# Kernel tuning notes

Measured on AMD Instinct MI355X. Metric: run time of the kernel, lower is better.

Reference implementation:

```python
import jax, jax.numpy as jnp
import numpy as np


def _jacobian_circulant(v):
    """Spatial Jacobian of a 3D vector field with circulant boundaries.

    v : (B, X, Y, Z, D) velocity field (channels last)
    returns J : (B, X, Y, Z, D, D) with J[..., i, j] = d v_i / d x_j,
    computed by central differences with wrap-around (circulant) bounds.
    """
    cols = []
    for j in range(3):
        ax = 1 + j  # spatial axis for coordinate j
        g = (jnp.roll(v, -1, axis=ax) - jnp.roll(v, 1, axis=ax)) * 0.5
        cols.append(g)
    return jnp.stack(cols, axis=-1)  # (B, X, Y, Z, D, D)


def _bracket(x, y):
    """Lie bracket of two velocity fields: [x, y] = J_x y - J_y x."""
    jx = _jacobian_circulant(x)
    jy = _jacobian_circulant(y)
    return (jnp.einsum('bxyzij,bxyzj->bxyzi', jx, y)
            - jnp.einsum('bxyzij,bxyzj->bxyzi', jy, x))


def _bch(x, y, trunc=2):
    """Truncated BCH series: z s.t. exp(z) = exp(x) o exp(y)."""
    z = x + y
    if trunc >= 2:
        z = z + 0.5 * _bracket(x, y)
    return z


def setup_inputs() -> dict:
    key = jax.random.key(0)
    k1, k2 = jax.random.split(key)
    B, D, X, Y, Z = 2, 3, 128, 128, 128
    left = jax.random.normal(k1, (B, D, X, Y, Z), dtype=jnp.float32)
    right = jax.random.normal(k2, (B, D, X, Y, Z), dtype=jnp.float32)
    return {"left": left, "right": right}


def reference(left, right):
    # (B, D, *shape) -> channels-last (B, *shape, D)
    l = jnp.moveaxis(left, 1, -1)
    r = jnp.moveaxis(right, 1, -1)
    v = _bch(l, r, trunc=2)
    return jnp.moveaxis(v, -1, 1)
```

## Files before the change

kernel.cpp:

```cpp
#include <hip/hip_runtime.h>


namespace {
constexpr int Xd = 128, Yd = 128, Zd = 128, Bd = 2, Dd = 3;
constexpr int Sd  = Xd * Yd * Zd;
constexpr int YZd = Yd * Zd;

__device__ inline float4 f4sub(float4 a, float4 b) {
    return make_float4(a.x - b.x, a.y - b.y, a.z - b.z, a.w - b.w);
}
__device__ inline float4 f4add(float4 a, float4 b) {
    return make_float4(a.x + b.x, a.y + b.y, a.z + b.z, a.w + b.w);
}
__device__ inline float4 f4mul(float4 a, float4 b) {
    return make_float4(a.x * b.x, a.y * b.y, a.z * b.z, a.w * b.w);
}
__device__ inline float4 f4fma(float4 a, float4 b, float4 c) {
    return make_float4(fmaf(a.x, b.x, c.x), fmaf(a.y, b.y, c.y),
                       fmaf(a.z, b.z, c.z), fmaf(a.w, b.w, c.w));
}
__device__ inline float4 f4fms(float4 a, float4 b, float4 c) {
    return make_float4(fmaf(-a.x, b.x, c.x), fmaf(-a.y, b.y, c.y),
                       fmaf(-a.z, b.z, c.z), fmaf(-a.w, b.w, c.w));
}
}

__global__ void __launch_bounds__(256)
bch_kernel(const float* __restrict__ L, const float* __restrict__ R,
           float* __restrict__ O)
{
    const int tid = blockIdx.x * 256 + threadIdx.x;
    const int z0  = (tid & 31) << 2;
    int t = tid >> 5;
    const int y = t & 127; t >>= 7;
    const int x = t & 127;
    const int b = t >> 7;

    const int base = b * (Dd * Sd) + x * YZd + y * Zd + z0;

    const int oxp = (((x + 1) & 127) - x) * YZd;
    const int oxm = (((x - 1) & 127) - x) * YZd;
    const int oyp = (((y + 1) & 127) - y) * Zd;
    const int oym = (((y - 1) & 127) - y) * Zd;
    const int ozm = ((z0 - 1) & 127) - z0;
    const int ozp = ((z0 + 4) & 127) - z0;

    float4 Lc[3], Rc[3];
#pragma unroll
    for (int d = 0; d < 3; ++d) {
        Lc[d] = *(const float4*)(L + base + d * Sd);
        Rc[d] = *(const float4*)(R + base + d * Sd);
    }

#pragma unroll
    for (int i = 0; i < 3; ++i) {
        const float* lp = L + base + i * Sd;
        const float* rp = R + base + i * Sd;

        float4 dl = f4sub(*(const float4*)(lp + oxp), *(const float4*)(lp + oxm));
        float4 dr = f4sub(*(const float4*)(rp + oxp), *(const float4*)(rp + oxm));
        float4 br = f4fms(dr, Lc[0], f4mul(dl, Rc[0]));

        dl = f4sub(*(const float4*)(lp + oyp), *(const float4*)(lp + oym));
        dr = f4sub(*(const float4*)(rp + oyp), *(const float4*)(rp + oym));
        br = f4fms(dr, Lc[1], f4fma(dl, Rc[1], br));

        const float lzm = lp[ozm], lzp = lp[ozp];
        const float rzm = rp[ozm], rzp = rp[ozp];
        dl = make_float4(Lc[i].y - lzm, Lc[i].z - Lc[i].x,
                         Lc[i].w - Lc[i].y, lzp - Lc[i].z);
        dr = make_float4(Rc[i].y - rzm, Rc[i].z - Rc[i].x,
                         Rc[i].w - Rc[i].y, rzp - Rc[i].z);
        br = f4fms(dr, Lc[2], f4fma(dl, Rc[2], br));

        float4 out = f4add(Lc[i], Rc[i]);
        const float4 q = make_float4(0.25f, 0.25f, 0.25f, 0.25f);
        out = f4fma(q, br, out);

        *(float4*)(O + base + i * Sd) = out;
    }
}

extern "C" void kernel_launch(void* const* d_in, const int* in_sizes, int n_in,
                              void* d_out, int out_size, void* d_ws, size_t ws_size,
                              hipStream_t stream)
{
    const float* L = (const float*)d_in[0];
    const float* R = (const float*)d_in[1];
    float*       O = (float*)d_out;

    const int nthreads = Bd * Xd * Yd * (Zd / 4);
    dim3 grid(nthreads / 256), block(256);
    bch_kernel<<<grid, block, 0, stream>>>(L, R, O);
}
```

Measured before the change: 152.2 us.

## March along y with register sliding window and warp shuffles for z neighbors

```diff
diff --git a/kernel.cpp b/kernel.cpp
--- a/kernel.cpp
+++ b/kernel.cpp
@@ -2,18 +2,17 @@
 
 
 namespace {
-constexpr int Xd = 128, Yd = 128, Zd = 128, Bd = 2, Dd = 3;
-constexpr int Sd  = Xd * Yd * Zd;
-constexpr int YZd = Yd * Zd;
+constexpr int NB = 2, ND = 3, NX = 128, NY = 128, NZ = 128;
+constexpr int XS = NY * NZ;
+constexpr int YSEG = 8;
+
+__device__ inline float4 ld4(const float* p) { return *(const float4*)p; }
 
 __device__ inline float4 f4sub(float4 a, float4 b) {
     return make_float4(a.x - b.x, a.y - b.y, a.z - b.z, a.w - b.w);
 }
 __device__ inline float4 f4add(float4 a, float4 b) {
     return make_float4(a.x + b.x, a.y + b.y, a.z + b.z, a.w + b.w);
-}
-__device__ inline float4 f4mul(float4 a, float4 b) {
-    return make_float4(a.x * b.x, a.y * b.y, a.z * b.z, a.w * b.w);
 }
 __device__ inline float4 f4fma(float4 a, float4 b, float4 c) {
     return make_float4(fmaf(a.x, b.x, c.x), fmaf(a.y, b.y, c.y),
@@ -23,61 +22,101 @@
     return make_float4(fmaf(-a.x, b.x, c.x), fmaf(-a.y, b.y, c.y),
                        fmaf(-a.z, b.z, c.z), fmaf(-a.w, b.w, c.w));
 }
+__device__ inline float4 f4mul(float4 a, float4 b) {
+    return make_float4(a.x * b.x, a.y * b.y, a.z * b.z, a.w * b.w);
+}
+
+__device__ inline float4 zderiv(float4 c, int srcm, int srcp) {
+    const float lw = __shfl(c.w, srcm, 64);
+    const float rx = __shfl(c.x, srcp, 64);
+    return make_float4(c.y - lw, c.z - c.x, c.w - c.y, rx - c.z);
+}
 }
 
 __global__ void __launch_bounds__(256)
 bch_kernel(const float* __restrict__ L, const float* __restrict__ R,
            float* __restrict__ O)
 {
-    const int tid = blockIdx.x * 256 + threadIdx.x;
-    const int z0  = (tid & 31) << 2;
-    int t = tid >> 5;
-    const int y = t & 127; t >>= 7;
-    const int x = t & 127;
-    const int b = t >> 7;
+    const int lane = threadIdx.x & 31;
+    const int g    = blockIdx.x * 8 + (threadIdx.x >> 5);
+    const int yseg = g & 15;
+    const int x    = (g >> 4) & 127;
+    const int b    = g >> 11;
+    const int z0   = lane << 2;
+    const int y0   = yseg * YSEG;
 
-    const int base = b * (Dd * Sd) + x * YZd + y * Zd + z0;
+    const int wl   = threadIdx.x & 63;
+    const int srcm = (wl & 32) | ((wl + 31) & 31);
+    const int srcp = (wl & 32) | ((wl + 1) & 31);
 
-    const int oxp = (((x + 1) & 127) - x) * YZd;
-    const int oxm = (((x - 1) & 127) - x) * YZd;
-    const int oyp = (((y + 1) & 127) - y) * Zd;
-    const int oym = (((y - 1) & 127) - y) * Zd;
-    const int ozm = ((z0 - 1) & 127) - z0;
-    const int ozp = ((z0 + 4) & 127) - z0;
-
-    float4 Lc[3], Rc[3];
+    int offc[3], offxp[3], offxm[3];
+    const int xp = (x + 1) & 127, xm = (x - 1) & 127;
 #pragma unroll
-    for (int d = 0; d < 3; ++d) {
-        Lc[d] = *(const float4*)(L + base + d * Sd);
-        Rc[d] = *(const float4*)(R + base + d * Sd);
+    for (int c = 0; c < 3; ++c) {
+        const int bc = (b * 3 + c) * NX;
+        offc[c]  = (bc + x)  * XS + z0;
+        offxp[c] = (bc + xp) * XS + z0;
+        offxm[c] = (bc + xm) * XS + z0;
     }
 
+    float4 Lm[3], Lc[3], Rm[3], Rc[3];
+    {
+        const int ymo = ((y0 + 127) & 127) * NZ;
+        const int yco = y0 * NZ;
 #pragma unroll
-    for (int i = 0; i < 3; ++i) {
-        const float* lp = L + base + i * Sd;
-        const float* rp = R + base + i * Sd;
+        for (int c = 0; c < 3; ++c) {
+            Lm[c] = ld4(L + offc[c] + ymo);
+            Rm[c] = ld4(R + offc[c] + ymo);
+            Lc[c] = ld4(L + offc[c] + yco);
+            Rc[c] = ld4(R + offc[c] + yco);
+        }
+    }
 
-        float4 dl = f4sub(*(const float4*)(lp + oxp), *(const float4*)(lp + oxm));
-        float4 dr = f4sub(*(const float4*)(rp + oxp), *(const float4*)(rp + oxm));
-        float4 br = f4fms(dr, Lc[0], f4mul(dl, Rc[0]));
+    for (int it = 0; it < YSEG; ++it) {
+        const int y  = y0 + it;
+        const int yr = y * NZ;
+        const int yp = ((y + 1) & 127) * NZ;
 
-        dl = f4sub(*(const float4*)(lp + oyp), *(const float4*)(lp + oym));
-        dr = f4sub(*(const float4*)(rp + oyp), *(const float4*)(rp + oym));
-        br = f4fms(dr, Lc[1], f4fma(dl, Rc[1], br));
+        float4 Lp[3], Rp[3], LxP[3], LxM[3], RxP[3], RxM[3];
+#pragma unroll
+        for (int c = 0; c < 3; ++c) {
+            Lp[c]  = ld4(L + offc[c]  + yp);
+            Rp[c]  = ld4(R + offc[c]  + yp);
+            LxP[c] = ld4(L + offxp[c] + yr);
+            LxM[c] = ld4(L + offxm[c] + yr);
+            RxP[c] = ld4(R + offxp[c] + yr);
+            RxM[c] = ld4(R + offxm[c] + yr);
+        }
 
-        const float lzm = lp[ozm], lzp = lp[ozp];
-        const float rzm = rp[ozm], rzp = rp[ozp];
-        dl = make_float4(Lc[i].y - lzm, Lc[i].z - Lc[i].x,
-                         Lc[i].w - Lc[i].y, lzp - Lc[i].z);
-        dr = make_float4(Rc[i].y - rzm, Rc[i].z - Rc[i].x,
-                         Rc[i].w - Rc[i].y, rzp - Rc[i].z);
-        br = f4fms(dr, Lc[2], f4fma(dl, Rc[2], br));
+        float4 dzL[3], dzR[3];
+#pragma unroll
+        for (int c = 0; c < 3; ++c) {
+            dzL[c] = zderiv(Lc[c], srcm, srcp);
+            dzR[c] = zderiv(Rc[c], srcm, srcp);
+        }
 
-        float4 out = f4add(Lc[i], Rc[i]);
-        const float4 q = make_float4(0.25f, 0.25f, 0.25f, 0.25f);
-        out = f4fma(q, br, out);
+#pragma unroll
+        for (int i = 0; i < 3; ++i) {
+            const float4 dxL = f4sub(LxP[i], LxM[i]);
+            const float4 dxR = f4sub(RxP[i], RxM[i]);
+            const float4 dyL = f4sub(Lp[i], Lm[i]);
+            const float4 dyR = f4sub(Rp[i], Rm[i]);
 
-        *(float4*)(O + base + i * Sd) = out;
+            float4 br = f4fms(dxR, Lc[0], f4mul(dxL, Rc[0]));
+            br = f4fms(dyR, Lc[1], f4fma(dyL, Rc[1], br));
+            br = f4fms(dzR[i], Lc[2], f4fma(dzL[i], Rc[2], br));
+
+            float4 out = f4add(Lc[i], Rc[i]);
+            const float4 q = make_float4(0.25f, 0.25f, 0.25f, 0.25f);
+            out = f4fma(q, br, out);
+            *(float4*)(O + offc[i] + yr) = out;
+        }
+
+#pragma unroll
+        for (int c = 0; c < 3; ++c) {
+            Lm[c] = Lc[c]; Lc[c] = Lp[c];
+            Rm[c] = Rc[c]; Rc[c] = Rp[c];
+        }
     }
 }
 
@@ -89,7 +128,6 @@
     const float* R = (const float*)d_in[1];
     float*       O = (float*)d_out;
 
-    const int nthreads = Bd * Xd * Yd * (Zd / 4);
-    dim3 grid(nthreads / 256), block(256);
+    dim3 grid(512), block(256);
     bch_kernel<<<grid, block, 0, stream>>>(L, R, O);
 }
```

Measured after the change: 163.4 us. 7.4% more time.
